# Optimization experiments

Measured on AMD Instinct MI355X. Metric: run time of the kernel, lower is better.

The kernel has to match this reference:

```python
import jax, jax.numpy as jnp
import numpy as np

B, T, I, H, O = 256, 512, 64, 256, 1

def setup_inputs() -> dict:
    key = jax.random.key(0)
    ks = jax.random.split(key, 7)
    s_ih = 1.0 / np.sqrt(H)
    return {
        "x": jax.random.normal(ks[0], (B, T, I), dtype=jnp.float32),
        "W_ih": jax.random.uniform(ks[1], (H, I), jnp.float32, -s_ih, s_ih),
        "W_hh": jax.random.uniform(ks[2], (H, H), jnp.float32, -s_ih, s_ih),
        "b_ih": jax.random.uniform(ks[3], (H,), jnp.float32, -s_ih, s_ih),
        "b_hh": jax.random.uniform(ks[4], (H,), jnp.float32, -s_ih, s_ih),
        "fc_W": jax.random.uniform(ks[5], (O, H), jnp.float32, -s_ih, s_ih),
        "fc_b": jax.random.uniform(ks[6], (O,), jnp.float32, -s_ih, s_ih),
    }

def reference(x, W_ih, W_hh, b_ih, b_hh, fc_W, fc_b):
    # PyTorch RNN (tanh): h_t = tanh(x_t W_ih^T + b_ih + h_{t-1} W_hh^T + b_hh)
    # Precompute the input projection for all timesteps in one GEMM: [B,T,H]
    xW = jnp.einsum('bti,hi->bth', x, W_ih) + (b_ih + b_hh)
    xW_t = jnp.transpose(xW, (1, 0, 2))  # time-major [T,B,H] for scan
    h0 = jnp.zeros((x.shape[0], W_hh.shape[0]), dtype=x.dtype)

    def step(h, xw_t):
        h_new = jnp.tanh(xw_t + h @ W_hh.T)
        return h_new, None

    h_last, _ = jax.lax.scan(step, h0, xW_t)
    return h_last @ fc_W.T + fc_b  # [B,O]
```

## Files before the change

### kernel.cpp

```cpp
#include <hip/hip_runtime.h>
#include <stdint.h>


#define RNN_B 256
#define RNN_T 512
#define RNN_I 64
#define RNN_H 256

#define STEP(RD, WR) \
  "ds_read_b128 v[0:3], "   RD " offset:0\n\t" \
  "ds_read_b128 v[4:7], "   RD " offset:16\n\t" \
  "ds_read_b128 v[8:11], "  RD " offset:32\n\t" \
  "ds_read_b128 v[12:15], " RD " offset:48\n\t" \
  "ds_read_b128 v[16:19], " RD " offset:64\n\t" \
  "ds_read_b128 v[20:23], " RD " offset:80\n\t" \
  "ds_read_b128 v[24:27], " RD " offset:96\n\t" \
  "ds_read_b128 v[28:31], " RD " offset:112\n\t" \
  "ds_read_b128 v[32:35], v55 offset:0\n\t" \
  "ds_read_b128 v[48:51], v55 offset:16\n\t" \
  "v_add_u32 v55, 0x100, v55\n\t" \
  "s_waitcnt lgkmcnt(6)\n\t" \
  "v_pk_mul_f32 v[36:37], v[0:1], v[64:65]\n\t" \
  "v_pk_mul_f32 v[38:39], v[0:1], v[96:97]\n\t" \
  "v_pk_mul_f32 v[40:41], v[0:1], v[128:129]\n\t" \
  "v_pk_mul_f32 v[42:43], v[0:1], v[160:161]\n\t" \
  "v_pk_fma_f32 v[36:37], v[2:3], v[66:67], v[36:37]\n\t" \
  "v_pk_fma_f32 v[38:39], v[2:3], v[98:99], v[38:39]\n\t" \
  "v_pk_fma_f32 v[40:41], v[2:3], v[130:131], v[40:41]\n\t" \
  "v_pk_fma_f32 v[42:43], v[2:3], v[162:163], v[42:43]\n\t" \
  "v_pk_fma_f32 v[36:37], v[4:5], v[68:69], v[36:37]\n\t" \
  "v_pk_fma_f32 v[38:39], v[4:5], v[100:101], v[38:39]\n\t" \
  "v_pk_fma_f32 v[40:41], v[4:5], v[132:133], v[40:41]\n\t" \
  "v_pk_fma_f32 v[42:43], v[4:5], v[164:165], v[42:43]\n\t" \
  "v_pk_fma_f32 v[36:37], v[6:7], v[70:71], v[36:37]\n\t" \
  "v_pk_fma_f32 v[38:39], v[6:7], v[102:103], v[38:39]\n\t" \
  "v_pk_fma_f32 v[40:41], v[6:7], v[134:135], v[40:41]\n\t" \
  "v_pk_fma_f32 v[42:43], v[6:7], v[166:167], v[42:43]\n\t" \
  "v_pk_fma_f32 v[36:37], v[8:9], v[72:73], v[36:37]\n\t" \
  "v_pk_fma_f32 v[38:39], v[8:9], v[104:105], v[38:39]\n\t" \
  "v_pk_fma_f32 v[40:41], v[8:9], v[136:137], v[40:41]\n\t" \
  "v_pk_fma_f32 v[42:43], v[8:9], v[168:169], v[42:43]\n\t" \
  "v_pk_fma_f32 v[36:37], v[10:11], v[74:75], v[36:37]\n\t" \
  "v_pk_fma_f32 v[38:39], v[10:11], v[106:107], v[38:39]\n\t" \
  "v_pk_fma_f32 v[40:41], v[10:11], v[138:139], v[40:41]\n\t" \
  "v_pk_fma_f32 v[42:43], v[10:11], v[170:171], v[42:43]\n\t" \
  "v_pk_fma_f32 v[36:37], v[12:13], v[76:77], v[36:37]\n\t" \
  "v_pk_fma_f32 v[38:39], v[12:13], v[108:109], v[38:39]\n\t" \
  "v_pk_fma_f32 v[40:41], v[12:13], v[140:141], v[40:41]\n\t" \
  "v_pk_fma_f32 v[42:43], v[12:13], v[172:173], v[42:43]\n\t" \
  "v_pk_fma_f32 v[36:37], v[14:15], v[78:79], v[36:37]\n\t" \
  "v_pk_fma_f32 v[38:39], v[14:15], v[110:111], v[38:39]\n\t" \
  "v_pk_fma_f32 v[40:41], v[14:15], v[142:143], v[40:41]\n\t" \
  "v_pk_fma_f32 v[42:43], v[14:15], v[174:175], v[42:43]\n\t" \
  "s_waitcnt lgkmcnt(2)\n\t" \
  "v_pk_fma_f32 v[36:37], v[16:17], v[80:81], v[36:37]\n\t" \
  "v_pk_fma_f32 v[38:39], v[16:17], v[112:113], v[38:39]\n\t" \
  "v_pk_fma_f32 v[40:41], v[16:17], v[144:145], v[40:41]\n\t" \
  "v_pk_fma_f32 v[42:43], v[16:17], v[176:177], v[42:43]\n\t" \
  "v_pk_fma_f32 v[36:37], v[18:19], v[82:83], v[36:37]\n\t" \
  "v_pk_fma_f32 v[38:39], v[18:19], v[114:115], v[38:39]\n\t" \
  "v_pk_fma_f32 v[40:41], v[18:19], v[146:147], v[40:41]\n\t" \
  "v_pk_fma_f32 v[42:43], v[18:19], v[178:179], v[42:43]\n\t" \
  "v_pk_fma_f32 v[36:37], v[20:21], v[84:85], v[36:37]\n\t" \
  "v_pk_fma_f32 v[38:39], v[20:21], v[116:117], v[38:39]\n\t" \
  "v_pk_fma_f32 v[40:41], v[20:21], v[148:149], v[40:41]\n\t" \
  "v_pk_fma_f32 v[42:43], v[20:21], v[180:181], v[42:43]\n\t" \
  "v_pk_fma_f32 v[36:37], v[22:23], v[86:87], v[36:37]\n\t" \
  "v_pk_fma_f32 v[38:39], v[22:23], v[118:119], v[38:39]\n\t" \
  "v_pk_fma_f32 v[40:41], v[22:23], v[150:151], v[40:41]\n\t" \
  "v_pk_fma_f32 v[42:43], v[22:23], v[182:183], v[42:43]\n\t" \
  "v_pk_fma_f32 v[36:37], v[24:25], v[88:89], v[36:37]\n\t" \
  "v_pk_fma_f32 v[38:39], v[24:25], v[120:121], v[38:39]\n\t" \
  "v_pk_fma_f32 v[40:41], v[24:25], v[152:153], v[40:41]\n\t" \
  "v_pk_fma_f32 v[42:43], v[24:25], v[184:185], v[42:43]\n\t" \
  "v_pk_fma_f32 v[36:37], v[26:27], v[90:91], v[36:37]\n\t" \
  "v_pk_fma_f32 v[38:39], v[26:27], v[122:123], v[38:39]\n\t" \
  "v_pk_fma_f32 v[40:41], v[26:27], v[154:155], v[40:41]\n\t" \
  "v_pk_fma_f32 v[42:43], v[26:27], v[186:187], v[42:43]\n\t" \
  "v_pk_fma_f32 v[36:37], v[28:29], v[92:93], v[36:37]\n\t" \
  "v_pk_fma_f32 v[38:39], v[28:29], v[124:125], v[38:39]\n\t" \
  "v_pk_fma_f32 v[40:41], v[28:29], v[156:157], v[40:41]\n\t" \
  "v_pk_fma_f32 v[42:43], v[28:29], v[188:189], v[42:43]\n\t" \
  "v_pk_fma_f32 v[36:37], v[30:31], v[94:95], v[36:37]\n\t" \
  "v_pk_fma_f32 v[38:39], v[30:31], v[126:127], v[38:39]\n\t" \
  "v_pk_fma_f32 v[40:41], v[30:31], v[158:159], v[40:41]\n\t" \
  "v_pk_fma_f32 v[42:43], v[30:31], v[190:191], v[42:43]\n\t" \
  "s_waitcnt lgkmcnt(0)\n\t" \
  "v_pk_fma_f32 v[36:37], v[32:33], v[192:193], v[36:37]\n\t" \
  "v_pk_fma_f32 v[38:39], v[32:33], v[200:201], v[38:39]\n\t" \
  "v_pk_fma_f32 v[40:41], v[32:33], v[208:209], v[40:41]\n\t" \
  "v_pk_fma_f32 v[42:43], v[32:33], v[216:217], v[42:43]\n\t" \
  "v_pk_fma_f32 v[36:37], v[34:35], v[194:195], v[36:37]\n\t" \
  "v_pk_fma_f32 v[38:39], v[34:35], v[202:203], v[38:39]\n\t" \
  "v_pk_fma_f32 v[40:41], v[34:35], v[210:211], v[40:41]\n\t" \
  "v_pk_fma_f32 v[42:43], v[34:35], v[218:219], v[42:43]\n\t" \
  "v_pk_fma_f32 v[36:37], v[48:49], v[196:197], v[36:37]\n\t" \
  "v_pk_fma_f32 v[38:39], v[48:49], v[204:205], v[38:39]\n\t" \
  "v_pk_fma_f32 v[40:41], v[48:49], v[212:213], v[40:41]\n\t" \
  "v_pk_fma_f32 v[42:43], v[48:49], v[220:221], v[42:43]\n\t" \
  "v_pk_fma_f32 v[36:37], v[50:51], v[198:199], v[36:37]\n\t" \
  "v_pk_fma_f32 v[38:39], v[50:51], v[206:207], v[38:39]\n\t" \
  "v_pk_fma_f32 v[40:41], v[50:51], v[214:215], v[40:41]\n\t" \
  "v_pk_fma_f32 v[42:43], v[50:51], v[222:223], v[42:43]\n\t" \
  "v_add_f32 v44, v36, v37\n\t" \
  "v_add_f32 v45, v38, v39\n\t" \
  "v_add_f32 v46, v40, v41\n\t" \
  "v_add_f32 v47, v42, v43\n\t" \
  "v_cndmask_b32 v52, v46, v44, %[m1]\n\t" \
  "v_cndmask_b32 v44, v44, v46, %[m1]\n\t" \
  "v_cndmask_b32 v53, v47, v45, %[m1]\n\t" \
  "v_cndmask_b32 v45, v45, v47, %[m1]\n\t" \
  "ds_bpermute_b32 v52, %[bp1], v52\n\t" \
  "ds_bpermute_b32 v53, %[bp1], v53\n\t" \
  "s_waitcnt lgkmcnt(0)\n\t" \
  "v_add_f32 v44, v44, v52\n\t" \
  "v_add_f32 v45, v45, v53\n\t" \
  "v_cndmask_b32 v52, v45, v44, %[m2]\n\t" \
  "v_cndmask_b32 v44, v44, v45, %[m2]\n\t" \
  "ds_bpermute_b32 v52, %[bp2], v52\n\t" \
  "s_waitcnt lgkmcnt(0)\n\t" \
  "v_add_f32 v44, v44, v52\n\t" \
  "ds_bpermute_b32 v52, %[bp4], v44\n\t" \
  "s_waitcnt lgkmcnt(0)\n\t" \
  "v_add_f32 v44, v44, v52\n\t" \
  "v_add_f32 v44, %[bias], v44\n\t" \
  "v_max_f32 v44, %[klo], v44\n\t" \
  "v_min_f32 v44, %[khi], v44\n\t" \
  "v_mul_f32 v44, %[km], v44\n\t" \
  "v_exp_f32 v53, v44\n\t" \
  "s_nop 1\n\t" \
  "v_subrev_f32 v54, 1.0, v53\n\t" \
  "v_add_f32 v53, 1.0, v53\n\t" \
  "v_rcp_f32 v53, v53\n\t" \
  "s_nop 1\n\t" \
  "v_mul_f32 v54, v54, v53\n\t" \
  "v_mov_b32 %[hj], v54\n\t" \
  "ds_write_b32 " WR ", v54\n\t" \
  "s_waitcnt lgkmcnt(0)\n\t" \
  "s_barrier\n\t"

__global__
__attribute__((amdgpu_flat_work_group_size(512, 512), amdgpu_waves_per_eu(2, 2)))
void rnn_fused_kernel(const float* __restrict__ x,
                      const float* __restrict__ W_ih,
                      const float* __restrict__ W_hh,
                      const float* __restrict__ b_ih,
                      const float* __restrict__ b_hh,
                      const float* __restrict__ fc_W,
                      const float* __restrict__ fc_b,
                      float* __restrict__ out)
{
    const int b   = blockIdx.x;
    const int tid = threadIdx.x;
    const int w   = tid >> 6;
    const int l   = tid & 63;
    const int g   = l >> 3;
    const int s   = l & 7;
    const int j0  = w * 32 + g * 4;

    __shared__ float hbuf[2][320];
    __shared__ float xt[32][RNN_I];
    __shared__ float red[8];

    const int   jjsel = ((s & 1) << 1) | ((s >> 1) & 1);
    const int   j_fin = j0 + jjsel;
    const int   jslot = j_fin + 4 * w;
    const int   wslot = (s < 4) ? jslot : (288 + (l & 31));
    const float bias2 = b_ih[j_fin] + b_hh[j_fin];
    const float fcw   = fc_W[j_fin];

    const uint32_t hb   = (uint32_t)(uintptr_t)&hbuf[0][0];
    const uint32_t xtb  = (uint32_t)(uintptr_t)&xt[0][0];
    const uint32_t hrd0 = hb + 144u * (uint32_t)s;
    const uint32_t hrd1 = hb + 1280u + 144u * (uint32_t)s;
    const uint32_t hwr0 = hb + 4u * (uint32_t)wslot;
    const uint32_t hwr1 = hb + 1280u + 4u * (uint32_t)wslot;
    const uint32_t xst  = xtb + 16u * (uint32_t)tid;
    const uint32_t xrd0 = xtb + 32u * (uint32_t)s;

    const uint32_t bp1 = (uint32_t)((l ^ 1) << 2);
    const uint32_t bp2 = (uint32_t)((l ^ 2) << 2);
    const uint32_t bp4 = (uint32_t)((l ^ 4) << 2);
    const unsigned long long m1 = __ballot(s & 1);
    const unsigned long long m2 = __ballot(s & 2);

    const float* whp = W_hh + (size_t)j0 * RNN_H + 32 * s;
    const float* wip = W_ih + (size_t)j0 * RNN_I + 8 * s;
    const float* xgp = x + (size_t)b * RNN_T * RNN_I + 4 * tid;
    const uint32_t whlo = (uint32_t)(uintptr_t)whp, whhi = (uint32_t)((uintptr_t)whp >> 32);
    const uint32_t wilo = (uint32_t)(uintptr_t)wip, wihi = (uint32_t)((uintptr_t)wip >> 32);
    const uint32_t xglo = (uint32_t)(uintptr_t)xgp, xghi = (uint32_t)((uintptr_t)xgp >> 32);

    if (tid < 320) hbuf[0][tid] = 0.0f;
    __syncthreads();

    float hj = 0.0f;
    int cntt, cnts, sadv;
    const float khi = 10.0f, klo = -10.0f, km = 2.8853900817779268f;

    asm volatile(
        "v_mov_b32 v56, %[whlo]\n\t"
        "v_mov_b32 v57, %[whhi]\n\t"
        "global_load_dwordx4 v[64:67],   v[56:57], off\n\t"
        "global_load_dwordx4 v[68:71],   v[56:57], off offset:16\n\t"
        "global_load_dwordx4 v[72:75],   v[56:57], off offset:32\n\t"
        "global_load_dwordx4 v[76:79],   v[56:57], off offset:48\n\t"
        "global_load_dwordx4 v[80:83],   v[56:57], off offset:64\n\t"
        "global_load_dwordx4 v[84:87],   v[56:57], off offset:80\n\t"
        "global_load_dwordx4 v[88:91],   v[56:57], off offset:96\n\t"
        "global_load_dwordx4 v[92:95],   v[56:57], off offset:112\n\t"
        "global_load_dwordx4 v[96:99],   v[56:57], off offset:1024\n\t"
        "global_load_dwordx4 v[100:103], v[56:57], off offset:1040\n\t"
        "global_load_dwordx4 v[104:107], v[56:57], off offset:1056\n\t"
        "global_load_dwordx4 v[108:111], v[56:57], off offset:1072\n\t"
        "global_load_dwordx4 v[112:115], v[56:57], off offset:1088\n\t"
        "global_load_dwordx4 v[116:119], v[56:57], off offset:1104\n\t"
        "global_load_dwordx4 v[120:123], v[56:57], off offset:1120\n\t"
        "global_load_dwordx4 v[124:127], v[56:57], off offset:1136\n\t"
        "global_load_dwordx4 v[128:131], v[56:57], off offset:2048\n\t"
        "global_load_dwordx4 v[132:135], v[56:57], off offset:2064\n\t"
        "global_load_dwordx4 v[136:139], v[56:57], off offset:2080\n\t"
        "global_load_dwordx4 v[140:143], v[56:57], off offset:2096\n\t"
        "global_load_dwordx4 v[144:147], v[56:57], off offset:2112\n\t"
        "global_load_dwordx4 v[148:151], v[56:57], off offset:2128\n\t"
        "global_load_dwordx4 v[152:155], v[56:57], off offset:2144\n\t"
        "global_load_dwordx4 v[156:159], v[56:57], off offset:2160\n\t"
        "global_load_dwordx4 v[160:163], v[56:57], off offset:3072\n\t"
        "global_load_dwordx4 v[164:167], v[56:57], off offset:3088\n\t"
        "global_load_dwordx4 v[168:171], v[56:57], off offset:3104\n\t"
        "global_load_dwordx4 v[172:175], v[56:57], off offset:3120\n\t"
        "global_load_dwordx4 v[176:179], v[56:57], off offset:3136\n\t"
        "global_load_dwordx4 v[180:183], v[56:57], off offset:3152\n\t"
        "global_load_dwordx4 v[184:187], v[56:57], off offset:3168\n\t"
        "global_load_dwordx4 v[188:191], v[56:57], off offset:3184\n\t"
        "v_mov_b32 v56, %[wilo]\n\t"
        "v_mov_b32 v57, %[wihi]\n\t"
        "global_load_dwordx4 v[192:195], v[56:57], off\n\t"
        "global_load_dwordx4 v[196:199], v[56:57], off offset:16\n\t"
        "global_load_dwordx4 v[200:203], v[56:57], off offset:256\n\t"
        "global_load_dwordx4 v[204:207], v[56:57], off offset:272\n\t"
        "global_load_dwordx4 v[208:211], v[56:57], off offset:512\n\t"
        "global_load_dwordx4 v[212:215], v[56:57], off offset:528\n\t"
        "global_load_dwordx4 v[216:219], v[56:57], off offset:768\n\t"
        "global_load_dwordx4 v[220:223], v[56:57], off offset:784\n\t"
        "v_mov_b32 v58, %[xglo]\n\t"
        "v_mov_b32 v59, %[xghi]\n\t"
        "global_load_dwordx4 v[60:63], v[58:59], off\n\t"
        "v_add_co_u32 v58, vcc, 0x2000, v58\n\t"
        "v_addc_co_u32 v59, vcc, 0, v59, vcc\n\t"
        "s_mov_b32 %[cntt], 16\n\t"
        "LTILE%=:\n\t"
        "s_waitcnt vmcnt(0)\n\t"
        "ds_write_b128 %[xst], v[60:63]\n\t"
        "global_load_dwordx4 v[60:63], v[58:59], off\n\t"
        "s_cmp_lg_u32 %[cntt], 2\n\t"
        "s_cselect_b32 %[sadv], 0x2000, 0\n\t"
        "v_add_co_u32 v58, vcc, %[sadv], v58\n\t"
        "v_addc_co_u32 v59, vcc, 0, v59, vcc\n\t"
        "v_mov_b32 v55, %[xrd0]\n\t"
        "s_waitcnt lgkmcnt(0)\n\t"
        "s_barrier\n\t"
        "s_mov_b32 %[cnts], 16\n\t"
        "LSTEP%=:\n\t"
        STEP("%[hrd0]", "%[hwr1]")
        STEP("%[hrd1]", "%[hwr0]")
        "s_sub_u32 %[cnts], %[cnts], 1\n\t"
        "s_cmp_lg_u32 %[cnts], 0\n\t"
        "s_cbranch_scc1 LSTEP%=\n\t"
        "s_sub_u32 %[cntt], %[cntt], 1\n\t"
        "s_cmp_lg_u32 %[cntt], 0\n\t"
        "s_cbranch_scc1 LTILE%=\n\t"
        "s_waitcnt vmcnt(0)\n\t"
        : [hj] "+v"(hj), [cntt] "=&s"(cntt), [cnts] "=&s"(cnts), [sadv] "=&s"(sadv)
        : [whlo] "v"(whlo), [whhi] "v"(whhi), [wilo] "v"(wilo), [wihi] "v"(wihi),
          [xglo] "v"(xglo), [xghi] "v"(xghi), [xst] "v"(xst), [xrd0] "v"(xrd0),
          [hrd0] "v"(hrd0), [hrd1] "v"(hrd1), [hwr0] "v"(hwr0), [hwr1] "v"(hwr1),
          [bp1] "v"(bp1), [bp2] "v"(bp2), [bp4] "v"(bp4), [bias] "v"(bias2),
          [m1] "s"(m1), [m2] "s"(m2),
          [khi] "s"(khi), [klo] "s"(klo), [km] "s"(km)
        : "memory", "vcc", "scc",
          "v0","v1","v2","v3","v4","v5","v6","v7","v8","v9",
          "v10","v11","v12","v13","v14","v15","v16","v17","v18","v19",
          "v20","v21","v22","v23","v24","v25","v26","v27","v28","v29",
          "v30","v31","v32","v33","v34","v35","v36","v37","v38","v39",
          "v40","v41","v42","v43","v44","v45","v46","v47","v48","v49",
          "v50","v51","v52","v53","v54","v55","v56","v57","v58","v59",
          "v60","v61","v62","v63","v64","v65","v66","v67","v68","v69",
          "v70","v71","v72","v73","v74","v75","v76","v77","v78","v79",
          "v80","v81","v82","v83","v84","v85","v86","v87","v88","v89",
          "v90","v91","v92","v93","v94","v95","v96","v97","v98","v99",
          "v100","v101","v102","v103","v104","v105","v106","v107","v108","v109",
          "v110","v111","v112","v113","v114","v115","v116","v117","v118","v119",
          "v120","v121","v122","v123","v124","v125","v126","v127","v128","v129",
          "v130","v131","v132","v133","v134","v135","v136","v137","v138","v139",
          "v140","v141","v142","v143","v144","v145","v146","v147","v148","v149",
          "v150","v151","v152","v153","v154","v155","v156","v157","v158","v159",
          "v160","v161","v162","v163","v164","v165","v166","v167","v168","v169",
          "v170","v171","v172","v173","v174","v175","v176","v177","v178","v179",
          "v180","v181","v182","v183","v184","v185","v186","v187","v188","v189",
          "v190","v191","v192","v193","v194","v195","v196","v197","v198","v199",
          "v200","v201","v202","v203","v204","v205","v206","v207","v208","v209",
          "v210","v211","v212","v213","v214","v215","v216","v217","v218","v219",
          "v220","v221","v222","v223");

    float term = (s < 4) ? hj * fcw : 0.0f;
    #pragma unroll
    for (int d = 1; d < 64; d <<= 1) term += __shfl_xor(term, d, 64);
    if (l == 0) red[w] = term;
    __syncthreads();
    if (tid == 0) {
        float sum = 0.f;
        #pragma unroll
        for (int ww = 0; ww < 8; ++ww) sum += red[ww];
        out[b] = sum + fc_b[0];
    }
}

extern "C" void kernel_launch(void* const* d_in, const int* in_sizes, int n_in,
                              void* d_out, int out_size, void* d_ws, size_t ws_size,
                              hipStream_t stream) {
    const float* x    = (const float*)d_in[0];
    const float* W_ih = (const float*)d_in[1];
    const float* W_hh = (const float*)d_in[2];
    const float* b_ih = (const float*)d_in[3];
    const float* b_hh = (const float*)d_in[4];
    const float* fc_W = (const float*)d_in[5];
    const float* fc_b = (const float*)d_in[6];
    float* out = (float*)d_out;

    rnn_fused_kernel<<<RNN_B, 512, 0, stream>>>(x, W_ih, W_hh, b_ih, b_hh, fc_W, fc_b, out);
}
```

Baseline: 342.8 us.

## Use DPP/swizzle for reduction, pad x tile, and finer-grained LDS waits

Replaces the ds_bpermute-based cross-lane reduction with DPP quad_perm moves for the xor-1 and xor-2 steps and a ds_swizzle for the xor-4 step. This removes LDS round trips and waits from the serial per-timestep critical path. The x staging tile gets a padded layout with a 68-float row stride plus an extra 16-byte skip, to avoid LDS bank conflicts on the reads. The single coarse lgkmcnt waits become a ladder of per-load waits so FMAs can start as each ds_read returns. The padded address maths must stay consistent with the write, read and advance offsets, or results will be silently wrong.

```diff
diff --git a/kernel.cpp b/kernel.cpp
--- a/kernel.cpp
+++ b/kernel.cpp
@@ -18,8 +18,8 @@
   "ds_read_b128 v[28:31], " RD " offset:112\n\t" \
   "ds_read_b128 v[32:35], v55 offset:0\n\t" \
   "ds_read_b128 v[48:51], v55 offset:16\n\t" \
-  "v_add_u32 v55, 0x100, v55\n\t" \
-  "s_waitcnt lgkmcnt(6)\n\t" \
+  "v_add_u32 v55, 0x110, v55\n\t" \
+  "s_waitcnt lgkmcnt(9)\n\t" \
   "v_pk_mul_f32 v[36:37], v[0:1], v[64:65]\n\t" \
   "v_pk_mul_f32 v[38:39], v[0:1], v[96:97]\n\t" \
   "v_pk_mul_f32 v[40:41], v[0:1], v[128:129]\n\t" \
@@ -28,6 +28,7 @@
   "v_pk_fma_f32 v[38:39], v[2:3], v[98:99], v[38:39]\n\t" \
   "v_pk_fma_f32 v[40:41], v[2:3], v[130:131], v[40:41]\n\t" \
   "v_pk_fma_f32 v[42:43], v[2:3], v[162:163], v[42:43]\n\t" \
+  "s_waitcnt lgkmcnt(8)\n\t" \
   "v_pk_fma_f32 v[36:37], v[4:5], v[68:69], v[36:37]\n\t" \
   "v_pk_fma_f32 v[38:39], v[4:5], v[100:101], v[38:39]\n\t" \
   "v_pk_fma_f32 v[40:41], v[4:5], v[132:133], v[40:41]\n\t" \
@@ -36,6 +37,7 @@
   "v_pk_fma_f32 v[38:39], v[6:7], v[102:103], v[38:39]\n\t" \
   "v_pk_fma_f32 v[40:41], v[6:7], v[134:135], v[40:41]\n\t" \
   "v_pk_fma_f32 v[42:43], v[6:7], v[166:167], v[42:43]\n\t" \
+  "s_waitcnt lgkmcnt(7)\n\t" \
   "v_pk_fma_f32 v[36:37], v[8:9], v[72:73], v[36:37]\n\t" \
   "v_pk_fma_f32 v[38:39], v[8:9], v[104:105], v[38:39]\n\t" \
   "v_pk_fma_f32 v[40:41], v[8:9], v[136:137], v[40:41]\n\t" \
@@ -44,6 +46,7 @@
   "v_pk_fma_f32 v[38:39], v[10:11], v[106:107], v[38:39]\n\t" \
   "v_pk_fma_f32 v[40:41], v[10:11], v[138:139], v[40:41]\n\t" \
   "v_pk_fma_f32 v[42:43], v[10:11], v[170:171], v[42:43]\n\t" \
+  "s_waitcnt lgkmcnt(6)\n\t" \
   "v_pk_fma_f32 v[36:37], v[12:13], v[76:77], v[36:37]\n\t" \
   "v_pk_fma_f32 v[38:39], v[12:13], v[108:109], v[38:39]\n\t" \
   "v_pk_fma_f32 v[40:41], v[12:13], v[140:141], v[40:41]\n\t" \
@@ -52,7 +55,7 @@
   "v_pk_fma_f32 v[38:39], v[14:15], v[110:111], v[38:39]\n\t" \
   "v_pk_fma_f32 v[40:41], v[14:15], v[142:143], v[40:41]\n\t" \
   "v_pk_fma_f32 v[42:43], v[14:15], v[174:175], v[42:43]\n\t" \
-  "s_waitcnt lgkmcnt(2)\n\t" \
+  "s_waitcnt lgkmcnt(5)\n\t" \
   "v_pk_fma_f32 v[36:37], v[16:17], v[80:81], v[36:37]\n\t" \
   "v_pk_fma_f32 v[38:39], v[16:17], v[112:113], v[38:39]\n\t" \
   "v_pk_fma_f32 v[40:41], v[16:17], v[144:145], v[40:41]\n\t" \
@@ -61,6 +64,7 @@
   "v_pk_fma_f32 v[38:39], v[18:19], v[114:115], v[38:39]\n\t" \
   "v_pk_fma_f32 v[40:41], v[18:19], v[146:147], v[40:41]\n\t" \
   "v_pk_fma_f32 v[42:43], v[18:19], v[178:179], v[42:43]\n\t" \
+  "s_waitcnt lgkmcnt(4)\n\t" \
   "v_pk_fma_f32 v[36:37], v[20:21], v[84:85], v[36:37]\n\t" \
   "v_pk_fma_f32 v[38:39], v[20:21], v[116:117], v[38:39]\n\t" \
   "v_pk_fma_f32 v[40:41], v[20:21], v[148:149], v[40:41]\n\t" \
@@ -69,6 +73,7 @@
   "v_pk_fma_f32 v[38:39], v[22:23], v[118:119], v[38:39]\n\t" \
   "v_pk_fma_f32 v[40:41], v[22:23], v[150:151], v[40:41]\n\t" \
   "v_pk_fma_f32 v[42:43], v[22:23], v[182:183], v[42:43]\n\t" \
+  "s_waitcnt lgkmcnt(3)\n\t" \
   "v_pk_fma_f32 v[36:37], v[24:25], v[88:89], v[36:37]\n\t" \
   "v_pk_fma_f32 v[38:39], v[24:25], v[120:121], v[38:39]\n\t" \
   "v_pk_fma_f32 v[40:41], v[24:25], v[152:153], v[40:41]\n\t" \
@@ -77,6 +82,7 @@
   "v_pk_fma_f32 v[38:39], v[26:27], v[122:123], v[38:39]\n\t" \
   "v_pk_fma_f32 v[40:41], v[26:27], v[154:155], v[40:41]\n\t" \
   "v_pk_fma_f32 v[42:43], v[26:27], v[186:187], v[42:43]\n\t" \
+  "s_waitcnt lgkmcnt(2)\n\t" \
   "v_pk_fma_f32 v[36:37], v[28:29], v[92:93], v[36:37]\n\t" \
   "v_pk_fma_f32 v[38:39], v[28:29], v[124:125], v[38:39]\n\t" \
   "v_pk_fma_f32 v[40:41], v[28:29], v[156:157], v[40:41]\n\t" \
@@ -85,7 +91,7 @@
   "v_pk_fma_f32 v[38:39], v[30:31], v[126:127], v[38:39]\n\t" \
   "v_pk_fma_f32 v[40:41], v[30:31], v[158:159], v[40:41]\n\t" \
   "v_pk_fma_f32 v[42:43], v[30:31], v[190:191], v[42:43]\n\t" \
-  "s_waitcnt lgkmcnt(0)\n\t" \
+  "s_waitcnt lgkmcnt(1)\n\t" \
   "v_pk_fma_f32 v[36:37], v[32:33], v[192:193], v[36:37]\n\t" \
   "v_pk_fma_f32 v[38:39], v[32:33], v[200:201], v[38:39]\n\t" \
   "v_pk_fma_f32 v[40:41], v[32:33], v[208:209], v[40:41]\n\t" \
@@ -94,6 +100,7 @@
   "v_pk_fma_f32 v[38:39], v[34:35], v[202:203], v[38:39]\n\t" \
   "v_pk_fma_f32 v[40:41], v[34:35], v[210:211], v[40:41]\n\t" \
   "v_pk_fma_f32 v[42:43], v[34:35], v[218:219], v[42:43]\n\t" \
+  "s_waitcnt lgkmcnt(0)\n\t" \
   "v_pk_fma_f32 v[36:37], v[48:49], v[196:197], v[36:37]\n\t" \
   "v_pk_fma_f32 v[38:39], v[48:49], v[204:205], v[38:39]\n\t" \
   "v_pk_fma_f32 v[40:41], v[48:49], v[212:213], v[40:41]\n\t" \
@@ -106,21 +113,24 @@
   "v_add_f32 v45, v38, v39\n\t" \
   "v_add_f32 v46, v40, v41\n\t" \
   "v_add_f32 v47, v42, v43\n\t" \
+   \
   "v_cndmask_b32 v52, v46, v44, %[m1]\n\t" \
   "v_cndmask_b32 v44, v44, v46, %[m1]\n\t" \
   "v_cndmask_b32 v53, v47, v45, %[m1]\n\t" \
   "v_cndmask_b32 v45, v45, v47, %[m1]\n\t" \
-  "ds_bpermute_b32 v52, %[bp1], v52\n\t" \
-  "ds_bpermute_b32 v53, %[bp1], v53\n\t" \
-  "s_waitcnt lgkmcnt(0)\n\t" \
+  "s_nop 1\n\t" \
+  "v_mov_b32_dpp v52, v52 quad_perm:[1,0,3,2] row_mask:0xf bank_mask:0xf\n\t" \
+  "v_mov_b32_dpp v53, v53 quad_perm:[1,0,3,2] row_mask:0xf bank_mask:0xf\n\t" \
   "v_add_f32 v44, v44, v52\n\t" \
   "v_add_f32 v45, v45, v53\n\t" \
+   \
   "v_cndmask_b32 v52, v45, v44, %[m2]\n\t" \
   "v_cndmask_b32 v44, v44, v45, %[m2]\n\t" \
-  "ds_bpermute_b32 v52, %[bp2], v52\n\t" \
-  "s_waitcnt lgkmcnt(0)\n\t" \
+  "s_nop 1\n\t" \
+  "v_mov_b32_dpp v52, v52 quad_perm:[2,3,0,1] row_mask:0xf bank_mask:0xf\n\t" \
   "v_add_f32 v44, v44, v52\n\t" \
-  "ds_bpermute_b32 v52, %[bp4], v44\n\t" \
+   \
+  "ds_swizzle_b32 v52, v44 offset:0x101F\n\t" \
   "s_waitcnt lgkmcnt(0)\n\t" \
   "v_add_f32 v44, v44, v52\n\t" \
   "v_add_f32 v44, %[bias], v44\n\t" \
@@ -159,7 +169,7 @@
     const int j0  = w * 32 + g * 4;
 
     __shared__ float hbuf[2][320];
-    __shared__ float xt[32][RNN_I];
+    __shared__ float xt[32 * 68];
     __shared__ float red[8];
 
     const int   jjsel = ((s & 1) << 1) | ((s >> 1) & 1);
@@ -170,17 +180,16 @@
     const float fcw   = fc_W[j_fin];
 
     const uint32_t hb   = (uint32_t)(uintptr_t)&hbuf[0][0];
-    const uint32_t xtb  = (uint32_t)(uintptr_t)&xt[0][0];
+    const uint32_t xtb  = (uint32_t)(uintptr_t)&xt[0];
     const uint32_t hrd0 = hb + 144u * (uint32_t)s;
     const uint32_t hrd1 = hb + 1280u + 144u * (uint32_t)s;
     const uint32_t hwr0 = hb + 4u * (uint32_t)wslot;
     const uint32_t hwr1 = hb + 1280u + 4u * (uint32_t)wslot;
-    const uint32_t xst  = xtb + 16u * (uint32_t)tid;
-    const uint32_t xrd0 = xtb + 32u * (uint32_t)s;
-
-    const uint32_t bp1 = (uint32_t)((l ^ 1) << 2);
-    const uint32_t bp2 = (uint32_t)((l ^ 2) << 2);
-    const uint32_t bp4 = (uint32_t)((l ^ 4) << 2);
+    const uint32_t xst  = xtb + 272u * (uint32_t)(tid >> 4)
+                              + 16u * (uint32_t)(tid & 15)
+                              + 16u * (uint32_t)((tid & 15) >> 3);
+    const uint32_t xrd0 = xtb + 32u * (uint32_t)s + 16u * (uint32_t)(s >> 2);
+
     const unsigned long long m1 = __ballot(s & 1);
     const unsigned long long m2 = __ballot(s & 2);
 
@@ -275,7 +284,7 @@
         : [whlo] "v"(whlo), [whhi] "v"(whhi), [wilo] "v"(wilo), [wihi] "v"(wihi),
           [xglo] "v"(xglo), [xghi] "v"(xghi), [xst] "v"(xst), [xrd0] "v"(xrd0),
           [hrd0] "v"(hrd0), [hrd1] "v"(hrd1), [hwr0] "v"(hwr0), [hwr1] "v"(hwr1),
-          [bp1] "v"(bp1), [bp2] "v"(bp2), [bp4] "v"(bp4), [bias] "v"(bias2),
+          [bias] "v"(bias2),
           [m1] "s"(m1), [m2] "s"(m2),
           [khi] "s"(khi), [klo] "s"(klo), [km] "s"(km)
         : "memory", "vcc", "scc",
```

Measured after the change: 321.6 us. 1.07x faster.
